# Optimization experiments

Measured on AMD Instinct MI355X. Metric: run time of the kernel, lower is better.

The kernel has to match this reference:

```python
import jax, jax.numpy as jnp
import numpy as np

COST_CLASS, COST_MASK, COST_DICE = 1.0, 1.0, 1.0
ALPHA, GAMMA = 0.25, 2.0


def setup_inputs() -> dict:
    key = jax.random.key(0)
    k1, k2, k3, k4 = jax.random.split(key, 4)
    B, Q, C, H, W, T, Hm, Wm = 2, 100, 134, 256, 256, 20, 512, 512
    return {
        "masks_queries_logits": jax.random.normal(k1, (B, Q, H, W), jnp.float32),
        "class_queries_logits": jax.random.normal(k2, (B, Q, C), jnp.float32),
        "mask_labels": jax.random.uniform(k3, (B, T, Hm, Wm), dtype=jnp.float32),
        "class_labels": jax.random.randint(k4, (B, T), 0, C),
    }


def _nearest_resize(x, H, W):
    # torch F.interpolate(mode='nearest'): src_idx = floor(dst_idx * in / out)
    Hi, Wi = x.shape[-2], x.shape[-1]
    ri = (jnp.arange(H) * Hi) // H
    ci = (jnp.arange(W) * Wi) // W
    return x[..., ri, :][..., ci]


def _cost_matrices(masks_queries_logits, class_queries_logits, mask_labels, class_labels):
    B, Q, H, W = masks_queries_logits.shape
    HW = H * W
    tgt = _nearest_resize(mask_labels, H, W)                       # [B,T,H,W]
    probs = jax.nn.softmax(class_queries_logits, axis=-1)          # [B,Q,C]
    # cost_class = -probs[:, labels]  -> [B,Q,T]
    cost_class = -jnp.take_along_axis(
        probs, jnp.broadcast_to(class_labels[:, None, :], (B, Q, class_labels.shape[1])), axis=2
    )
    x = masks_queries_logits.reshape(B, Q, HW)                     # [B,Q,HW]
    lab = tgt.reshape(B, -1, HW)                                   # [B,T,HW]
    p = jax.nn.sigmoid(x)
    ce_pos = jax.nn.softplus(-x)   # BCEWithLogits(target=1)
    ce_neg = jax.nn.softplus(x)    # BCEWithLogits(target=0)
    focal_pos = ALPHA * (1.0 - p) ** GAMMA * ce_pos
    focal_neg = (1.0 - ALPHA) * p ** GAMMA * ce_neg
    cost_mask = (jnp.einsum('bqk,btk->bqt', focal_pos, lab)
                 + jnp.einsum('bqk,btk->bqt', focal_neg, 1.0 - lab)) / HW
    numer = 2.0 * jnp.einsum('bqk,btk->bqt', p, lab)
    denom = p.sum(-1)[:, :, None] + lab.sum(-1)[:, None, :]
    cost_dice = 1.0 - (numer + 1.0) / (denom + 1.0)
    return COST_MASK * cost_mask + COST_CLASS * cost_class + COST_DICE * cost_dice


def _hungarian(cost):
    # Exact O(n^3) Hungarian (Jonker-Volgenant style potentials), numpy on host.
    # Zero-pads to square like the torch code; dummy cols all-zero so the real
    # assignment equals the rectangular optimum.
    n_rows, n_cols = cost.shape
    n = max(n_rows, n_cols)
    a = np.zeros((n + 1, n + 1), dtype=np.float64)
    a[1:n_rows + 1, 1:n_cols + 1] = cost
    u = np.zeros(n + 1); v = np.zeros(n + 1)
    p = np.zeros(n + 1, dtype=np.int64)
    way = np.zeros(n + 1, dtype=np.int64)
    for i in range(1, n + 1):
        p[0] = i; j0 = 0
        minv = np.full(n + 1, np.inf)
        used = np.zeros(n + 1, dtype=bool)
        while True:
            used[j0] = True
            i0 = p[j0]
            cur = a[i0, 1:] - u[i0] - v[1:]
            free = ~used[1:]
            upd = free & (cur < minv[1:])
            minv[1:][upd] = cur[upd]
            way[1:][upd] = j0
            cand = np.where(free, minv[1:], np.inf)
            j1 = int(np.argmin(cand)) + 1
            delta = cand[j1 - 1]
            u[p[used]] += delta
            v[used] -= delta
            minv[1:][free] -= delta
            j0 = j1
            if p[j0] == 0:
                break
        while j0:
            j1 = way[j0]
            p[j0] = p[j1]
            j0 = j1
    rows, cols = [], []
    for j in range(1, n_cols + 1):
        r = p[j] - 1
        if 0 <= r < n_rows:
            rows.append(r); cols.append(j - 1)
    rows = np.asarray(rows, dtype=np.int64)
    cols = np.asarray(cols, dtype=np.int64)
    order = np.argsort(rows)  # torch impl emits pairs in ascending row order
    return rows[order], cols[order]


def reference(masks_queries_logits, class_queries_logits, mask_labels, class_labels):
    cost = _cost_matrices(masks_queries_logits, class_queries_logits, mask_labels, class_labels)
    cost_np = np.asarray(jax.device_get(cost), dtype=np.float64)  # [B,Q,T]
    pairs = [np.stack(_hungarian(c)) for c in cost_np]            # each [2, min(Q,T)]
    return jnp.asarray(np.stack(pairs), dtype=jnp.int32)          # [B, 2, T]
```

## Files before the change

### kernel.cpp

```cpp
#include <hip/hip_runtime.h>
#include <hip/hip_bf16.h>
#include <math.h>

#define HW_   65536
#define B_    2
#define Q_    100
#define C_    134
#define T_    20
#define NHUN  100
#define MT_   7
#define KSB   128
#define BKCH  512
#define PREC  1088
#define CPAD  21

typedef __attribute__((ext_vector_type(8))) short bf16x8;
typedef __attribute__((ext_vector_type(4))) float f32x4;

#define LABPS_OFF  0
#define CC_OFF     512
#define COST_OFF   4608
#define BASE_END   8704
#define LABT_HI_F  BASE_END
#define PART_OFF   (LABT_HI_F + 1310720)
#define CSUM_OFF   (PART_OFF + B_ * KSB * MT_ * PREC)
#define WS_END_F   (CSUM_OFF + B_ * MT_ * 1056)

__device__ inline unsigned short f2bf(float f) {
    unsigned int u = __builtin_bit_cast(unsigned int, f);
    u += 0x7FFFu + ((u >> 16) & 1u);
    return (unsigned short)(u >> 16);
}
__device__ inline float softplusf(float x) {
    float ax = fabsf(x);
    return fmaxf(x, 0.0f) + log1pf(expf(-ax));
}

__global__ void lab_prep_kernel(const float* __restrict__ ml, unsigned short* __restrict__ labT,
                                float* __restrict__ lab_ps, int writeT) {
    int b = blockIdx.x, t = blockIdx.y, ksl = blockIdx.z;
    int tid = threadIdx.x;
    const float* src = ml + (size_t)(b * T_ + t) * 262144;
    size_t dst = ((size_t)(b * T_ + t)) << 16;
    float acc = 0.f;
    for (int it = 0; it < 8; ++it) {
        int k = ksl * 8192 + it * 1024 + tid * 4;
        int r = k >> 8, c = k & 255;
        const float* s = src + r * 1024 + 2 * c;
        float4 u = *(const float4*)s;
        float4 w = *(const float4*)(s + 4);
        float v[4] = {u.x, u.z, w.x, w.z};
        unsigned short h[4];
#pragma unroll
        for (int e = 0; e < 4; ++e) { h[e] = f2bf(v[e]); acc += v[e]; }
        if (writeT) *(ushort4*)(labT + dst + k) = make_ushort4(h[0], h[1], h[2], h[3]);
    }
    for (int off = 32; off > 0; off >>= 1) acc += __shfl_down(acc, off);
    __shared__ float sb[4];
    int wid = tid >> 6, lane = tid & 63;
    if (lane == 0) sb[wid] = acc;
    __syncthreads();
    if (tid == 0) lab_ps[(b * T_ + t) * 8 + ksl] = sb[0] + sb[1] + sb[2] + sb[3];
}

__global__ void class_cost_kernel(const float* __restrict__ cl, const int* __restrict__ labels,
                                  float* __restrict__ cc) {
    int bq  = blockIdx.x;
    int b   = bq / Q_;
    int tid = threadIdx.x;
    __shared__ float sl[C_];
    const float* src = cl + (size_t)bq * C_;
    for (int c = tid; c < C_; c += 64) sl[c] = src[c];
    __syncthreads();
    float mx = -INFINITY;
    for (int c = tid; c < C_; c += 64) mx = fmaxf(mx, sl[c]);
    for (int off = 32; off > 0; off >>= 1) mx = fmaxf(mx, __shfl_xor(mx, off));
    float se = 0.f;
    for (int c = tid; c < C_; c += 64) se += expf(sl[c] - mx);
    for (int off = 32; off > 0; off >>= 1) se += __shfl_xor(se, off);
    float inv = 1.0f / se;
    if (tid < T_) {
        int lbl = labels[b * T_ + tid];
        cc[bq * T_ + tid] = -expf(sl[lbl] - mx) * inv;
    }
}

__global__ __launch_bounds__(256, 4) void focal_mfma_kernel(
        const float* __restrict__ mq, const unsigned short* __restrict__ labT,
        float* __restrict__ part) {
    int idx = blockIdx.x;
    int mt  = idx % MT_;
    int rem = idx / MT_;
    int ks  = rem % KSB;
    int b   = rem / KSB;
    int tid  = threadIdx.x;
    int wave = tid >> 6, lane = tid & 63;
    int lg = lane >> 4, lr = lane & 15;

    int q = mt * 16 + lr;
    bool qok = (q < Q_);
    const float* xrow = mq + ((size_t)(b * Q_ + (qok ? q : 0)) << 16);
    int koff = ks * BKCH + wave * 128 + lg * 8;

    const unsigned short* b1 = labT + (((size_t)(b * T_ + lr)) << 16);
    const unsigned short* b2 = labT + (((size_t)(b * T_ + 16 + (lr & 3))) << 16);
    bool n2row = (lr < 4);

    bf16x8 zer;
#pragma unroll
    for (int e = 0; e < 8; ++e) zer[e] = 0;

    float4 a0[4], a1[4];
    bf16x8 bfrag1[4], bfrag2[4];
#pragma unroll
    for (int kk = 0; kk < 4; ++kk) {
        int kb = koff + kk * 32;
        a0[kk] = *(const float4*)(xrow + kb);
        a1[kk] = *(const float4*)(xrow + kb + 4);
        bfrag1[kk] = *(const bf16x8*)(b1 + kb);
        bfrag2[kk] = n2row ? *(const bf16x8*)(b2 + kb) : zer;
    }

    f32x4 accD0 = {0,0,0,0}, accD1 = {0,0,0,0};
    f32x4 accP0 = {0,0,0,0}, accP1 = {0,0,0,0};
    float F = 0.f, P = 0.f;

#pragma unroll
    for (int kk = 0; kk < 4; ++kk) {
        float xv[8] = {a0[kk].x, a0[kk].y, a0[kk].z, a0[kk].w,
                       a1[kk].x, a1[kk].y, a1[kk].z, a1[kk].w};
        bf16x8 dh, ph;
#pragma unroll
        for (int e = 0; e < 8; ++e) {
            float x  = xv[e];
            float ax = fabsf(x);
            float a  = __expf(-ax);
            float rr = 1.0f / (1.0f + a);
            float p  = (x >= 0.f) ? rr : a * rr;
            float om = (x >= 0.f) ? a * rr : rr;
            float l1 = __logf(1.0f + a);
            float spn = fmaxf(-x, 0.f) + l1;
            float spp = spn + x;
            float fp = 0.25f * om * om * spn;
            float fn = 0.75f * p * p * spp;
            F += fn; P += p;
            dh[e] = (short)f2bf(fp - fn);
            ph[e] = (short)f2bf(p);
        }
        accD0 = __builtin_amdgcn_mfma_f32_16x16x32_bf16(dh, bfrag1[kk], accD0, 0, 0, 0);
        accD1 = __builtin_amdgcn_mfma_f32_16x16x32_bf16(dh, bfrag2[kk], accD1, 0, 0, 0);
        accP0 = __builtin_amdgcn_mfma_f32_16x16x32_bf16(ph, bfrag1[kk], accP0, 0, 0, 0);
        accP1 = __builtin_amdgcn_mfma_f32_16x16x32_bf16(ph, bfrag2[kk], accP1, 0, 0, 0);
    }

    F += __shfl_down(F, 32); F += __shfl_down(F, 16);
    P += __shfl_down(P, 32); P += __shfl_down(P, 16);

    __shared__ float red[4][4][64][4];
    __shared__ float fpb[4][2][16];
#pragma unroll
    for (int r = 0; r < 4; ++r) {
        red[wave][0][lane][r] = accD0[r];
        red[wave][1][lane][r] = accD1[r];
        red[wave][2][lane][r] = accP0[r];
        red[wave][3][lane][r] = accP1[r];
    }
    if (lane < 16) { fpb[wave][0][lane] = F; fpb[wave][1][lane] = P; }
    __syncthreads();
    if (tid < 256) {
        int e4 = tid;
        int f  = e4 >> 6;
        int l2 = e4 & 63;
        float4 s;
        s.x = red[0][f][l2][0] + red[1][f][l2][0] + red[2][f][l2][0] + red[3][f][l2][0];
        s.y = red[0][f][l2][1] + red[1][f][l2][1] + red[2][f][l2][1] + red[3][f][l2][1];
        s.z = red[0][f][l2][2] + red[1][f][l2][2] + red[2][f][l2][2] + red[3][f][l2][2];
        s.w = red[0][f][l2][3] + red[1][f][l2][3] + red[2][f][l2][3] + red[3][f][l2][3];
        *(float4*)(part + (size_t)idx * PREC + e4 * 4) = s;
    }
    if (tid < 16)
        part[(size_t)idx * PREC + 1024 + tid] =
            fpb[0][0][tid] + fpb[1][0][tid] + fpb[2][0][tid] + fpb[3][0][tid];
    else if (tid < 32) {
        int l = tid - 16;
        part[(size_t)idx * PREC + 1040 + l] =
            fpb[0][1][l] + fpb[1][1][l] + fpb[2][1][l] + fpb[3][1][l];
    }
}

__global__ __launch_bounds__(256) void reduce_part_kernel(const float* __restrict__ part,
                                                          float* __restrict__ Csum) {
    int bm   = blockIdx.x;
    int mt   = bm % MT_;
    int b    = bm / MT_;
    int tid  = threadIdx.x;
    int epos = tid & 31;
    int grp  = tid >> 5;
    int e    = blockIdx.y * 32 + epos;

    const float* base = part + (size_t)((b * KSB) * MT_ + mt) * PREC + e;
    float s = 0.f;
    for (int k = 0; k < 16; ++k) {
        s += base[(size_t)(grp * 16 + k) * MT_ * PREC];
    }
    __shared__ float red[8][33];
    red[grp][epos] = s;
    __syncthreads();
    if (tid < 32) {
        float tot = 0.f;
        for (int g = 0; g < 8; ++g) tot += red[g][tid];
        Csum[(size_t)bm * 1056 + e] = tot;
    }
}

__global__ __launch_bounds__(320) void compose_kernel(
        const float* __restrict__ Csum, const float* __restrict__ cl,
        const int* __restrict__ labels, const float* __restrict__ lab_ps,
        float* __restrict__ cost) {
    int bm = blockIdx.x;
    int mt = bm % MT_;
    int b  = bm / MT_;
    int tid = threadIdx.x;
    int q0 = mt * 16;

    __shared__ float sl[16][136];
    __shared__ float mx[16], se[16];
    __shared__ int   lbl[T_];
    for (int e = tid; e < 16 * C_; e += 320) {
        int qm = e / C_, c = e % C_;
        int q = q0 + qm;
        sl[qm][c] = (q < Q_) ? cl[(size_t)(b * Q_ + q) * C_ + c] : 0.f;
    }
    if (tid < T_) lbl[tid] = labels[b * T_ + tid];
    __syncthreads();
    if (tid < 16) {
        float m = -INFINITY;
        for (int c = 0; c < C_; ++c) m = fmaxf(m, sl[tid][c]);
        float s = 0.f;
        for (int c = 0; c < C_; ++c) s += expf(sl[tid][c] - m);
        mx[tid] = m; se[tid] = s;
    }
    __syncthreads();

    int qm = tid / T_, t = tid % T_;
    int q = q0 + qm;
    if (qm < 16 && q < Q_) {
        const float* C = Csum + (size_t)bm * 1056;
        int nt   = t >> 4;
        int lane = ((qm >> 2) << 4) | (t & 15);
        int reg  = qm & 3;
        float Sd = C[(0 + nt) * 256 + lane * 4 + reg];
        float Sp = C[(2 + nt) * 256 + lane * 4 + reg];
        float F  = C[1024 + qm];
        float P  = C[1040 + qm];
        float L = 0.f;
        for (int s8 = 0; s8 < 8; ++s8) L += lab_ps[(b * T_ + t) * 8 + s8];
        float ccv = -expf(sl[qm][lbl[t]] - mx[qm]) / se[qm];
        float cm = (Sd + F) * (1.0f / (float)HW_);
        float cd = 1.0f - (2.0f * Sp + 1.0f) / (P + L + 1.0f);
        cost[(size_t)(b * Q_ + q) * T_ + t] = cm + cd + ccv;
    }
}

__global__ __launch_bounds__(1024) void mask_cost_mono_kernel(
        const float* __restrict__ mq, const float* __restrict__ ml,
        const float* __restrict__ cc, const float* __restrict__ lab_ps,
        float* __restrict__ cost) {
    int bq  = blockIdx.x;
    int b   = bq / Q_;
    int tid = threadIdx.x;
    const float* xb  = mq + (size_t)bq * HW_;
    const float* mlb = ml + (size_t)b * T_ * 262144;
    float s1[T_], s2[T_];
#pragma unroll
    for (int t = 0; t < T_; ++t) { s1[t] = 0.f; s2[t] = 0.f; }
    float F = 0.f, P = 0.f;
    for (int k = tid; k < HW_; k += 1024) {
        int i = k >> 8, j = k & 255;
        float x = xb[k];
        float p = 1.0f / (1.0f + expf(-x));
        float spn = softplusf(-x);
        float spp = softplusf(x);
        float om = 1.0f - p;
        float fp = 0.25f * om * om * spn;
        float fn = 0.75f * p * p * spp;
        F += fn; P += p;
        float diff = fp - fn;
        int off0 = i * 1024 + 2 * j;
#pragma unroll
        for (int t = 0; t < T_; ++t) {
            float lab = mlb[t * 262144 + off0];
            s1[t] = fmaf(diff, lab, s1[t]);
            s2[t] = fmaf(p,    lab, s2[t]);
        }
    }
    __shared__ float sbuf[16][42];
    int wid = tid >> 6, lane = tid & 63;
#pragma unroll
    for (int t = 0; t < T_; ++t) {
        for (int off = 32; off > 0; off >>= 1) {
            s1[t] += __shfl_down(s1[t], off);
            s2[t] += __shfl_down(s2[t], off);
        }
    }
    for (int off = 32; off > 0; off >>= 1) { F += __shfl_down(F, off); P += __shfl_down(P, off); }
    if (lane == 0) {
#pragma unroll
        for (int t = 0; t < T_; ++t) { sbuf[wid][t] = s1[t]; sbuf[wid][T_ + t] = s2[t]; }
        sbuf[wid][40] = F; sbuf[wid][41] = P;
    }
    __syncthreads();
    if (tid < T_) {
        float S1 = 0.f, S2 = 0.f, Fs = 0.f, Ps = 0.f;
        for (int w = 0; w < 16; ++w) {
            S1 += sbuf[w][tid]; S2 += sbuf[w][T_ + tid];
            Fs += sbuf[w][40];  Ps += sbuf[w][41];
        }
        float L = 0.f;
        for (int sl = 0; sl < 8; ++sl) L += lab_ps[(b * T_ + tid) * 8 + sl];
        float cm = (S1 + Fs) * (1.0f / (float)HW_);
        float cd = 1.0f - (2.0f * S2 + 1.0f) / (Ps + L + 1.0f);
        cost[bq * T_ + tid] = cm + cd + cc[bq * T_ + tid];
    }
}

__global__ __launch_bounds__(64) void hungarian_kernel(const float* __restrict__ cost,
                                                       int* __restrict__ out) {
    int b    = blockIdx.x;
    int lane = threadIdx.x;

    __shared__ float csh[Q_ * CPAD];
    __shared__ int   psh[NHUN + 1];

    for (int j = lane; j < Q_; j += 64) {
#pragma unroll
        for (int t = 0; t < T_; ++t)
            csh[j * CPAD + t] = cost[b * Q_ * T_ + j * T_ + t];
    }
    __syncthreads();

    const int ja = lane;
    const int jb = lane + 64;
    const bool ja_ok = (ja >= 1);
    const bool jb_ok = (jb <= NHUN);

    int   p_a = 0, p_b = 0;
    float v_a = 0.f, v_b = 0.f;
    float u_reg = 0.f;

    for (int i = 1; i <= T_; ++i) {
        float ca = ja_ok ? csh[(ja - 1) * CPAD + (i - 1)] : INFINITY;
        float cb = jb_ok ? csh[(jb - 1) * CPAD + (i - 1)] : INFINITY;
        float vmin = fminf(ca, cb);
        for (int off = 32; off > 0; off >>= 1)
            vmin = fminf(vmin, __shfl_xor(vmin, off));
        unsigned long long ba = __ballot(ca == vmin);
        int j1 = ba ? (__ffsll(ba) - 1) : (__ffsll(__ballot(cb == vmin)) - 1 + 64);
        if (lane == i) u_reg = vmin;
        int pj = __shfl((j1 < 64) ? p_a : p_b, j1 & 63);
        if (pj == 0) {
            if (j1 < 64) { if (lane == j1) p_a = i; }
            else         { if (lane == j1 - 64) p_b = i; }
        }
    }

    for (int i = 1; i <= T_; ++i) {
        bool mine = (p_a == i) || (p_b == i);
        if (__ballot(mine)) continue;

        float m_a = INFINITY, m_b = INFINITY;
        int   way_a = 0, way_b = 0;
        bool  us_a = false, us_b = false;
        bool  in_tree = (lane == i);
        int   j0 = 0, jf;

        while (true) {
            int i0 = (j0 == 0) ? i : __shfl((j0 < 64) ? p_a : p_b, j0 & 63);
            if (lane == i0) in_tree = true;
            float ui0 = __shfl(u_reg, i0);
            if (ja == j0) us_a = true;
            if (jb == j0) us_b = true;
            bool fa = ja_ok && !us_a;
            bool fb = jb_ok && !us_b;
            if (fa) {
                float cur = csh[(ja - 1) * CPAD + (i0 - 1)] - ui0 - v_a;
                if (cur < m_a) { m_a = cur; way_a = j0; }
            }
            if (fb) {
                float cur = csh[(jb - 1) * CPAD + (i0 - 1)] - ui0 - v_b;
                if (cur < m_b) { m_b = cur; way_b = j0; }
            }
            float ca = fa ? m_a : INFINITY;
            float cb = fb ? m_b : INFINITY;
            float vmin = fminf(ca, cb);
            for (int off = 32; off > 0; off >>= 1)
                vmin = fminf(vmin, __shfl_xor(vmin, off));
            unsigned long long ba = __ballot(ca == vmin);
            int j1 = ba ? (__ffsll(ba) - 1) : (__ffsll(__ballot(cb == vmin)) - 1 + 64);
            float delta = vmin;
            if (us_a) v_a -= delta; else m_a -= delta;
            if (us_b) v_b -= delta; else m_b -= delta;
            if (in_tree) u_reg += delta;
            j0 = j1;
            int pj0 = __shfl((j0 < 64) ? p_a : p_b, j0 & 63);
            if (pj0 == 0) { jf = j0; break; }
        }
        int jj = jf;
        while (jj) {
            int wv = __shfl((jj < 64) ? way_a : way_b, jj & 63);
            int pn = (wv == 0) ? i : __shfl((wv < 64) ? p_a : p_b, wv & 63);
            if (jj < 64) { if (lane == jj) p_a = pn; }
            else         { if (lane == jj - 64) p_b = pn; }
            jj = wv;
        }
    }

    if (ja_ok) psh[ja] = p_a;
    if (jb_ok) psh[jb] = p_b;
    if (lane == 0) psh[0] = 0;
    __syncthreads();
    if (lane == 0) {
        int* ob = out + b * 2 * T_;
        int k = 0;
        for (int j = 1; j <= NHUN; ++j) {
            if (psh[j] != 0) { ob[k] = j - 1; ob[T_ + k] = psh[j] - 1; ++k; }
        }
    }
}

extern "C" void kernel_launch(void* const* d_in, const int* in_sizes, int n_in,
                              void* d_out, int out_size, void* d_ws, size_t ws_size,
                              hipStream_t stream) {
    const float* mq     = (const float*)d_in[0];
    const float* cl     = (const float*)d_in[1];
    const float* ml     = (const float*)d_in[2];
    const int*   labels = (const int*)d_in[3];
    int* out = (int*)d_out;
    float* ws = (float*)d_ws;

    float* lab_ps = ws + LABPS_OFF;
    float* cc     = ws + CC_OFF;
    float* cost   = ws + COST_OFF;

    size_t need = (size_t)WS_END_F * 4;

    if (ws_size >= need) {
        unsigned short* labT = (unsigned short*)(ws + LABT_HI_F);
        float* part = ws + PART_OFF;
        float* Csum = ws + CSUM_OFF;
        hipLaunchKernelGGL(lab_prep_kernel,   dim3(B_, T_, 8), dim3(256), 0, stream,
                           ml, labT, lab_ps, 1);
        hipLaunchKernelGGL(focal_mfma_kernel, dim3(B_ * KSB * MT_), dim3(256), 0, stream,
                           mq, labT, part);
        hipLaunchKernelGGL(reduce_part_kernel, dim3(B_ * MT_, 33), dim3(256), 0, stream,
                           part, Csum);
        hipLaunchKernelGGL(compose_kernel,    dim3(B_ * MT_),  dim3(320), 0, stream,
                           Csum, cl, labels, lab_ps, cost);
    } else {
        hipLaunchKernelGGL(lab_prep_kernel,   dim3(B_, T_, 8), dim3(256), 0, stream,
                           ml, (unsigned short*)ws, lab_ps, 0);
        hipLaunchKernelGGL(class_cost_kernel, dim3(B_ * Q_),   dim3(64),  0, stream, cl, labels, cc);
        hipLaunchKernelGGL(mask_cost_mono_kernel, dim3(B_ * Q_), dim3(1024), 0, stream,
                           mq, ml, cc, lab_ps, cost);
    }
    hipLaunchKernelGGL(hungarian_kernel, dim3(B_), dim3(64), 0, stream, cost, out);
}
```

Before: 70.13 us.

## Stage focal-loss activations and labels through swizzled LDS before MFMA

```diff
diff --git a/kernel.cpp b/kernel.cpp
--- a/kernel.cpp
+++ b/kernel.cpp
@@ -85,7 +85,7 @@
     }
 }
 
-__global__ __launch_bounds__(256, 4) void focal_mfma_kernel(
+__global__ __launch_bounds__(256, 3) void focal_mfma_kernel(
         const float* __restrict__ mq, const unsigned short* __restrict__ labT,
         float* __restrict__ part) {
     int idx = blockIdx.x;
@@ -97,67 +97,92 @@
     int wave = tid >> 6, lane = tid & 63;
     int lg = lane >> 4, lr = lane & 15;
 
-    int q = mt * 16 + lr;
-    bool qok = (q < Q_);
-    const float* xrow = mq + ((size_t)(b * Q_ + (qok ? q : 0)) << 16);
-    int koff = ks * BKCH + wave * 128 + lg * 8;
-
-    const unsigned short* b1 = labT + (((size_t)(b * T_ + lr)) << 16);
-    const unsigned short* b2 = labT + (((size_t)(b * T_ + 16 + (lr & 3))) << 16);
-    bool n2row = (lr < 4);
-
-    bf16x8 zer;
-#pragma unroll
-    for (int e = 0; e < 8; ++e) zer[e] = 0;
-
-    float4 a0[4], a1[4];
-    bf16x8 bfrag1[4], bfrag2[4];
-#pragma unroll
-    for (int kk = 0; kk < 4; ++kk) {
-        int kb = koff + kk * 32;
-        a0[kk] = *(const float4*)(xrow + kb);
-        a1[kk] = *(const float4*)(xrow + kb + 4);
-        bfrag1[kk] = *(const bf16x8*)(b1 + kb);
-        bfrag2[kk] = n2row ? *(const bf16x8*)(b2 + kb) : zer;
-    }
-
-    f32x4 accD0 = {0,0,0,0}, accD1 = {0,0,0,0};
-    f32x4 accP0 = {0,0,0,0}, accP1 = {0,0,0,0};
-    float F = 0.f, P = 0.f;
-
-#pragma unroll
-    for (int kk = 0; kk < 4; ++kk) {
-        float xv[8] = {a0[kk].x, a0[kk].y, a0[kk].z, a0[kk].w,
-                       a1[kk].x, a1[kk].y, a1[kk].z, a1[kk].w};
-        bf16x8 dh, ph;
-#pragma unroll
-        for (int e = 0; e < 8; ++e) {
-            float x  = xv[e];
+    __shared__ __align__(16) char smem[53504];
+
+    for (int i = 0; i < 5; ++i) {
+        int t  = wave + 4 * i;
+        int k0 = lane * 8;
+        bf16x8 v = *(const bf16x8*)(labT + (((size_t)(b * T_ + t)) << 16) + ks * BKCH + k0);
+        int byte = 32768 + t * 1024 + (((k0 >> 3) ^ (t & 7)) << 4);
+        *(bf16x8*)(smem + byte) = v;
+    }
+
+    float Fr[4], Pr[4];
+#pragma unroll
+    for (int rr = 0; rr < 4; ++rr) { Fr[rr] = 0.f; Pr[rr] = 0.f; }
+#pragma unroll
+    for (int i = 0; i < 8; ++i) {
+        int rr   = i >> 1;
+        int r    = wave * 4 + rr;
+        int half = i & 1;
+        int k0   = half * 256 + lane * 4;
+        int q    = mt * 16 + r;
+        bool qok = (q < Q_);
+        const float* xr = mq + ((size_t)(b * Q_ + (qok ? q : 0)) << 16) + ks * BKCH;
+        float4 xv = *(const float4*)(xr + k0);
+        unsigned short dh[4], ph[4];
+        float Fs = 0.f, Ps = 0.f;
+#pragma unroll
+        for (int e = 0; e < 4; ++e) {
+            float x  = (&xv.x)[e];
             float ax = fabsf(x);
             float a  = __expf(-ax);
-            float rr = 1.0f / (1.0f + a);
-            float p  = (x >= 0.f) ? rr : a * rr;
-            float om = (x >= 0.f) ? a * rr : rr;
+            float rcp = 1.0f / (1.0f + a);
+            float p  = (x >= 0.f) ? rcp : a * rcp;
+            float om = (x >= 0.f) ? a * rcp : rcp;
             float l1 = __logf(1.0f + a);
             float spn = fmaxf(-x, 0.f) + l1;
             float spp = spn + x;
             float fp = 0.25f * om * om * spn;
             float fn = 0.75f * p * p * spp;
-            F += fn; P += p;
-            dh[e] = (short)f2bf(fp - fn);
-            ph[e] = (short)f2bf(p);
-        }
-        accD0 = __builtin_amdgcn_mfma_f32_16x16x32_bf16(dh, bfrag1[kk], accD0, 0, 0, 0);
-        accD1 = __builtin_amdgcn_mfma_f32_16x16x32_bf16(dh, bfrag2[kk], accD1, 0, 0, 0);
-        accP0 = __builtin_amdgcn_mfma_f32_16x16x32_bf16(ph, bfrag1[kk], accP0, 0, 0, 0);
-        accP1 = __builtin_amdgcn_mfma_f32_16x16x32_bf16(ph, bfrag2[kk], accP1, 0, 0, 0);
-    }
-
-    F += __shfl_down(F, 32); F += __shfl_down(F, 16);
-    P += __shfl_down(P, 32); P += __shfl_down(P, 16);
-
-    __shared__ float red[4][4][64][4];
-    __shared__ float fpb[4][2][16];
+            Fs += fn; Ps += p;
+            dh[e] = f2bf(fp - fn);
+            ph[e] = f2bf(p);
+        }
+        Fr[rr] += Fs; Pr[rr] += Ps;
+        if ((mt == 6) && (r == 4)) {
+            dh[0] = dh[1] = dh[2] = dh[3] = 0x3F80;
+            ph[0] = ph[1] = ph[2] = ph[3] = 0x3F80;
+        }
+        uint2 dv, pv;
+        dv.x = (unsigned)dh[0] | ((unsigned)dh[1] << 16);
+        dv.y = (unsigned)dh[2] | ((unsigned)dh[3] << 16);
+        pv.x = (unsigned)ph[0] | ((unsigned)ph[1] << 16);
+        pv.y = (unsigned)ph[2] | ((unsigned)ph[3] << 16);
+        int byte = r * 1024 + (((k0 >> 3) ^ (r & 7)) << 4) + ((k0 & 7) * 2);
+        *(uint2*)(smem + byte)         = dv;
+        *(uint2*)(smem + 16384 + byte) = pv;
+    }
+    __syncthreads();
+
+    f32x4 accD0 = {0,0,0,0}, accD1 = {0,0,0,0};
+    f32x4 accP0 = {0,0,0,0}, accP1 = {0,0,0,0};
+    bf16x8 zer;
+#pragma unroll
+    for (int e = 0; e < 8; ++e) zer[e] = 0;
+#pragma unroll
+    for (int kk = 0; kk < 4; ++kk) {
+        int k  = wave * 128 + kk * 32 + lg * 8;
+        int ab = lr * 1024 + (((k >> 3) ^ (lr & 7)) << 4);
+        bf16x8 dh = *(const bf16x8*)(smem + ab);
+        bf16x8 ph = *(const bf16x8*)(smem + 16384 + ab);
+        int t1 = lr;
+        bf16x8 f1 = *(const bf16x8*)(smem + 32768 + t1 * 1024 + (((k >> 3) ^ (t1 & 7)) << 4));
+        bf16x8 f2 = zer;
+        if (lr < 4) {
+            int t2 = 16 + lr;
+            f2 = *(const bf16x8*)(smem + 32768 + t2 * 1024 + (((k >> 3) ^ (t2 & 7)) << 4));
+        }
+        accD0 = __builtin_amdgcn_mfma_f32_16x16x32_bf16(dh, f1, accD0, 0, 0, 0);
+        accD1 = __builtin_amdgcn_mfma_f32_16x16x32_bf16(dh, f2, accD1, 0, 0, 0);
+        accP0 = __builtin_amdgcn_mfma_f32_16x16x32_bf16(ph, f1, accP0, 0, 0, 0);
+        accP1 = __builtin_amdgcn_mfma_f32_16x16x32_bf16(ph, f2, accP1, 0, 0, 0);
+    }
+    __syncthreads();
+
+    float (*red)[4][64][4] = (float (*)[4][64][4])smem;
+    float* fpF = (float*)(smem + 16384);
+    float* fpP = (float*)(smem + 16384 + 64);
 #pragma unroll
     for (int r = 0; r < 4; ++r) {
         red[wave][0][lane][r] = accD0[r];
@@ -165,9 +190,17 @@
         red[wave][2][lane][r] = accP0[r];
         red[wave][3][lane][r] = accP1[r];
     }
-    if (lane < 16) { fpb[wave][0][lane] = F; fpb[wave][1][lane] = P; }
-    __syncthreads();
-    if (tid < 256) {
+#pragma unroll
+    for (int rr = 0; rr < 4; ++rr) {
+        float f = Fr[rr], p = Pr[rr];
+        for (int off = 32; off > 0; off >>= 1) {
+            f += __shfl_down(f, off);
+            p += __shfl_down(p, off);
+        }
+        if (lane == 0) { fpF[wave * 4 + rr] = f; fpP[wave * 4 + rr] = p; }
+    }
+    __syncthreads();
+    {
         int e4 = tid;
         int f  = e4 >> 6;
         int l2 = e4 & 63;
@@ -179,13 +212,9 @@
         *(float4*)(part + (size_t)idx * PREC + e4 * 4) = s;
     }
     if (tid < 16)
-        part[(size_t)idx * PREC + 1024 + tid] =
-            fpb[0][0][tid] + fpb[1][0][tid] + fpb[2][0][tid] + fpb[3][0][tid];
-    else if (tid < 32) {
-        int l = tid - 16;
-        part[(size_t)idx * PREC + 1040 + l] =
-            fpb[0][1][l] + fpb[1][1][l] + fpb[2][1][l] + fpb[3][1][l];
-    }
+        part[(size_t)idx * PREC + 1024 + tid] = fpF[tid];
+    else if (tid < 32)
+        part[(size_t)idx * PREC + 1040 + (tid - 16)] = fpP[tid - 16];
 }
 
 __global__ __launch_bounds__(256) void reduce_part_kernel(const float* __restrict__ part,
@@ -200,9 +229,8 @@
 
     const float* base = part + (size_t)((b * KSB) * MT_ + mt) * PREC + e;
     float s = 0.f;
-    for (int k = 0; k < 16; ++k) {
+    for (int k = 0; k < 16; ++k)
         s += base[(size_t)(grp * 16 + k) * MT_ * PREC];
-    }
     __shared__ float red[8][33];
     red[grp][epos] = s;
     __syncthreads();
```

After: 74.23 us. 1.06x slower.
